# Optimization experiments

Measured on AMD Instinct MI355X. Metric: run time of the kernel, lower is better.

Reference implementation:

```python
import jax, jax.numpy as jnp
import numpy as np

K = 512
DIM = 64


def setup_inputs() -> dict:
    key = jax.random.key(0)
    kx, ke = jax.random.split(key)
    x = jax.random.normal(kx, (64, 64, 32, 32), dtype=jnp.float32)  # (b, d, h, w)
    codebook = jax.random.normal(ke, (K, DIM), dtype=jnp.float32)  # nn.Embedding weight
    return {"x": x, "codebook": codebook}


def reference(x, codebook):
    b, d, h, w = x.shape
    # (b, d, h*w) -> (b, h*w, d)
    flat = jnp.transpose(x.reshape(b, d, h * w), (0, 2, 1))  # (b, n, d)
    x2 = jnp.sum(flat * flat, axis=-1, keepdims=True)              # (b, n, 1)
    e2 = jnp.sum(codebook * codebook, axis=-1)                     # (k,)
    xe = jnp.einsum('bnd,kd->bnk', flat, codebook)                 # (b, n, k)
    dist = x2 - 2.0 * xe + e2                                      # (b, n, k)
    idx = jnp.argmin(dist, axis=-1)                                # (b, n)
    quant = codebook[idx]                                          # (b, n, d) gather
    # straight-through estimator
    quant_st = flat + jax.lax.stop_gradient(quant - flat)
    out = jnp.transpose(quant_st, (0, 2, 1)).reshape(b, d, h, w)
    return out
```

## Files before the change

kernel.cpp:

```cpp
#include <hip/hip_runtime.h>

#define KCODES 512
#define DIM    64
#define NVEC   65536
#define TAU    0.05f

typedef __attribute__((ext_vector_type(8))) short   short8;
typedef __attribute__((ext_vector_type(4))) float   f32x4;

static __device__ __forceinline__ unsigned f2bfu(float f) {
    unsigned u = __builtin_bit_cast(unsigned, f);
    u += 0x7fffu + ((u >> 16) & 1u);
    return u >> 16;
}

__global__ void prep_kernel(const float* __restrict__ cb,
                            unsigned short* __restrict__ cbh,
                            unsigned short* __restrict__ cbl,
                            float* __restrict__ e2q) {
    const int k = blockIdx.x, d = threadIdx.x;
    const int e = k * DIM + d;
    float v = cb[e];
    unsigned u = __builtin_bit_cast(unsigned, v);
    float hi = __builtin_bit_cast(float, u & 0xFFFF0000u);
    cbh[e] = (unsigned short)(u >> 16);
    cbl[e] = (unsigned short)f2bfu(v - hi);
    double p = (double)v * (double)v;
#pragma unroll
    for (int off = 32; off > 0; off >>= 1) p += __shfl_down(p, off, 64);
    if (d == 0) e2q[k] = (float)(0.5 * p + 256.0);
}

__launch_bounds__(128, 2)
__global__ void vq_main(const float* __restrict__ x,
                        const float* __restrict__ cb,
                        const unsigned short* __restrict__ cbh,
                        const unsigned short* __restrict__ cbl,
                        const float* __restrict__ e2q,
                        float* __restrict__ out) {
    __shared__ unsigned short sAh[2][4096];
    __shared__ unsigned short sAl[2][4096];
    __shared__ float sE2[KCODES];
    __shared__ int   s_i1[64], s_i2[64], s_flag[64], s_win[64];

    const int tid  = threadIdx.x;
    const int wave = tid >> 6;
    const int lane = tid & 63;
    const int quad = lane >> 4;
    const int l16  = lane & 15;

    const int v0    = blockIdx.x * 64;
    const int b     = v0 >> 10;
    const int nbase = v0 & 1023;
    const float* xb = x + (size_t)b * 65536;

    short8 stg[8];
#pragma unroll
    for (int r = 0; r < 8; ++r) {
        const int idx = tid + r * 128;
        const int q  = idx & 511;
        const int c  = q >> 3, qd = q & 7;
        const unsigned short* src = (idx < 512 ? cbh : cbl) + (size_t)c * 64 + qd * 8;
        stg[r] = *(const short8*)src;
    }

    short8 Bh[2][2], Bl[2][2];
#pragma unroll
    for (int nt = 0; nt < 2; ++nt) {
        const int n_g = nbase + wave * 32 + nt * 16 + l16;
#pragma unroll
        for (int ko = 0; ko < 2; ++ko) {
#pragma unroll
            for (int j = 0; j < 8; ++j) {
                const int d = quad * 8 + j + ko * 32;
                float f = -xb[(size_t)d * 1024 + n_g];
                unsigned u = __builtin_bit_cast(unsigned, f);
                float hi = __builtin_bit_cast(float, u & 0xFFFF0000u);
                Bh[nt][ko][j] = (short)(u >> 16);
                Bl[nt][ko][j] = (short)f2bfu(f - hi);
            }
        }
    }

    *(f32x4*)(sE2 + tid * 4) = *(const f32x4*)(e2q + tid * 4);
#pragma unroll
    for (int r = 0; r < 8; ++r) {
        const int idx = tid + r * 128;
        const int q  = idx & 511;
        const int c  = q >> 3, qd = q & 7;
        unsigned short* dst = (idx < 512 ? sAh[0] : sAl[0]) + (qd * 64 + c) * 8;
        *(short8*)dst = stg[r];
    }
    __syncthreads();

    float f1[2] = {1e30f, 1e30f}, f2_[2] = {1e30f, 1e30f};
    int   i1[2] = {0, 0},         i2_[2] = {0, 0};

#pragma unroll 1
    for (int s = 0; s < 8; ++s) {
        if (s < 7) {
#pragma unroll
            for (int r = 0; r < 8; ++r) {
                const int idx = tid + r * 128;
                const int q  = idx & 511;
                const int c  = q >> 3, qd = q & 7;
                const unsigned short* src =
                    (idx < 512 ? cbh : cbl) + (size_t)((s + 1) * 64 + c) * 64 + qd * 8;
                stg[r] = *(const short8*)src;
            }
        }

        const unsigned short* bh = sAh[s & 1];
        const unsigned short* bl = sAl[s & 1];
#pragma unroll
        for (int st = 0; st < 4; ++st) {
            const int cbase = s * 64 + st * 16;
            short8 Ah0 = *(const short8*)(bh + ( quad      * 64 + st * 16 + l16) * 8);
            short8 Ah1 = *(const short8*)(bh + ((quad + 4) * 64 + st * 16 + l16) * 8);
            short8 Al0 = *(const short8*)(bl + ( quad      * 64 + st * 16 + l16) * 8);
            short8 Al1 = *(const short8*)(bl + ((quad + 4) * 64 + st * 16 + l16) * 8);
            f32x4  e2v = *(const f32x4*)(sE2 + cbase + quad * 4);

#pragma unroll
            for (int nt = 0; nt < 2; ++nt) {
                f32x4 acc = e2v;
                acc = __builtin_amdgcn_mfma_f32_16x16x32_bf16(Ah0, Bh[nt][0], acc, 0, 0, 0);
                acc = __builtin_amdgcn_mfma_f32_16x16x32_bf16(Ah1, Bh[nt][1], acc, 0, 0, 0);
                acc = __builtin_amdgcn_mfma_f32_16x16x32_bf16(Ah0, Bl[nt][0], acc, 0, 0, 0);
                acc = __builtin_amdgcn_mfma_f32_16x16x32_bf16(Ah1, Bl[nt][1], acc, 0, 0, 0);
                acc = __builtin_amdgcn_mfma_f32_16x16x32_bf16(Al0, Bh[nt][0], acc, 0, 0, 0);
                acc = __builtin_amdgcn_mfma_f32_16x16x32_bf16(Al1, Bh[nt][1], acc, 0, 0, 0);
#pragma unroll
                for (int r = 0; r < 4; ++r) {
                    float dd = acc[r];
                    int   id = cbase + quad * 4 + r;
                    bool  c1 = dd < f1[nt];
                    bool  c2 = dd < f2_[nt];
                    i2_[nt] = c1 ? i1[nt] : (c2 ? id : i2_[nt]);
                    f2_[nt] = fminf(fmaxf(f1[nt], dd), f2_[nt]);
                    i1[nt]  = c1 ? id : i1[nt];
                    f1[nt]  = fminf(f1[nt], dd);
                }
            }
        }

        if (s < 7) {
#pragma unroll
            for (int r = 0; r < 8; ++r) {
                const int idx = tid + r * 128;
                const int q  = idx & 511;
                const int c  = q >> 3, qd = q & 7;
                unsigned short* dst =
                    (idx < 512 ? sAh[(s + 1) & 1] : sAl[(s + 1) & 1]) + (qd * 64 + c) * 8;
                *(short8*)dst = stg[r];
            }
        }
        __syncthreads();
    }

#pragma unroll
    for (int nt = 0; nt < 2; ++nt) {
        float F1 = f1[nt], F2 = f2_[nt];
        int   I1 = i1[nt], I2 = i2_[nt];
#pragma unroll
        for (int delta = 16; delta <= 32; delta <<= 1) {
            float of1 = __shfl_xor(F1, delta, 64);
            int   oi1 = __shfl_xor(I1, delta, 64);
            float of2 = __shfl_xor(F2, delta, 64);
            int   oi2 = __shfl_xor(I2, delta, 64);
            bool o1_first = (of1 < F1) || (of1 == F1 && oi1 < I1);
            if (o1_first) {
                bool keep = (F1 < of2) || (F1 == of2 && I1 < oi2);
                F2 = keep ? F1 : of2;
                I2 = keep ? I1 : oi2;
                F1 = of1; I1 = oi1;
            } else {
                bool o1_second = (of1 < F2) || (of1 == F2 && oi1 < I2);
                if (o1_second) { F2 = of1; I2 = oi1; }
            }
        }
        if (quad == 0) {
            const int vl = wave * 32 + nt * 16 + l16;
            s_win[vl]  = I1;
            s_i1[vl]   = I1;
            s_i2[vl]   = I2;
            s_flag[vl] = (F2 - F1) < TAU;
        }
    }
    __syncthreads();

    {
        const int vec = tid >> 1, sub = tid & 1;
        if (s_flag[vec]) {
            const int i1c = s_i1[vec], i2c = s_i2[vec];
            const float* xr = xb + nbase + vec;
            const float* r1 = cb + (size_t)i1c * DIM;
            const float* r2 = cb + (size_t)i2c * DIM;
            double D1 = 0.0, D2 = 0.0;
#pragma unroll 4
            for (int i = 0; i < 32; ++i) {
                const int d = sub + 2 * i;
                double xd = (double)xr[(size_t)d * 1024];
                double t1 = xd - (double)r1[d]; D1 += t1 * t1;
                double t2 = xd - (double)r2[d]; D2 += t2 * t2;
            }
            D1 += __shfl_down(D1, 1, 64);
            D2 += __shfl_down(D2, 1, 64);
            if (sub == 0) {
                if (D2 < D1 || (D2 == D1 && i2c < i1c)) s_win[vec] = i2c;
            }
        }
    }
    __syncthreads();

    {
        const int n    = tid & 63;
        const int dgrp = tid >> 6;
        const float4* crow = (const float4*)(cb + (size_t)s_win[n] * DIM);
        float* op = out + (size_t)b * 65536 + nbase + n;
#pragma unroll
        for (int i = 0; i < 8; ++i) {
            const int d0 = dgrp * 32 + i * 4;
            float4 val = crow[d0 >> 2];
            op[(size_t)(d0 + 0) * 1024] = val.x;
            op[(size_t)(d0 + 1) * 1024] = val.y;
            op[(size_t)(d0 + 2) * 1024] = val.z;
            op[(size_t)(d0 + 3) * 1024] = val.w;
        }
    }
}

extern "C" void kernel_launch(void* const* d_in, const int* in_sizes, int n_in,
                              void* d_out, int out_size, void* d_ws, size_t ws_size,
                              hipStream_t stream) {
    const float* x  = (const float*)d_in[0];
    const float* cb = (const float*)d_in[1];
    float* out = (float*)d_out;

    unsigned short* cbh = (unsigned short*)d_ws;
    unsigned short* cbl = cbh + KCODES * DIM;
    float*          e2q = (float*)(cbl + KCODES * DIM);

    prep_kernel<<<KCODES, 64, 0, stream>>>(cb, cbh, cbl, e2q);
    vq_main<<<NVEC / 64, 128, 0, stream>>>(x, cb, cbh, cbl, e2q, out);
}
```

Baseline: 106.6 us.

## Pre-tile codebook in LDS order and use four waves per 64-vector block

The prep kernel now writes the bf16 hi/lo codebook directly in the shared-memory tile order, so the main kernel stages it with plain contiguous 16-byte copies and no index shuffling. The main kernel goes from 128 to 256 threads per block, with each wave handling one 16-vector tile instead of two. Codebook staging, the refinement pass and the output write are split across the four waves. This is meant to raise the number of resident waves and spread the staging cost, at the price of each wave reusing its A-fragment LDS reads across fewer MFMAs.

```diff
diff --git a/kernel.cpp b/kernel.cpp
--- a/kernel.cpp
+++ b/kernel.cpp
@@ -15,31 +15,46 @@
 }
 
 __global__ void prep_kernel(const float* __restrict__ cb,
-                            unsigned short* __restrict__ cbh,
-                            unsigned short* __restrict__ cbl,
+                            unsigned short* __restrict__ cbt,
                             float* __restrict__ e2q) {
-    const int k = blockIdx.x, d = threadIdx.x;
-    const int e = k * DIM + d;
-    float v = cb[e];
-    unsigned u = __builtin_bit_cast(unsigned, v);
-    float hi = __builtin_bit_cast(float, u & 0xFFFF0000u);
-    cbh[e] = (unsigned short)(u >> 16);
-    cbl[e] = (unsigned short)f2bfu(v - hi);
-    double p = (double)v * (double)v;
-#pragma unroll
-    for (int off = 32; off > 0; off >>= 1) p += __shfl_down(p, off, 64);
-    if (d == 0) e2q[k] = (float)(0.5 * p + 256.0);
-}
-
-__launch_bounds__(128, 2)
+    if (blockIdx.x < 128) {
+        const int g   = blockIdx.x * 64 + threadIdx.x;
+        const int s   = g >> 10;
+        const int rem = g & 1023;
+        const int h   = rem >> 9;
+        const int qd  = (rem >> 6) & 7;
+        const int cl  = rem & 63;
+        const float* src = cb + (size_t)(s * 64 + cl) * DIM + qd * 8;
+        short8 v;
+#pragma unroll
+        for (int j = 0; j < 8; ++j) {
+            float f = src[j];
+            unsigned u = __builtin_bit_cast(unsigned, f);
+            if (h == 0) {
+                v[j] = (short)(u >> 16);
+            } else {
+                float hi = __builtin_bit_cast(float, u & 0xFFFF0000u);
+                v[j] = (short)f2bfu(f - hi);
+            }
+        }
+        *(short8*)(cbt + (size_t)g * 8) = v;
+    } else {
+        const int k = blockIdx.x - 128;
+        float v = cb[k * DIM + threadIdx.x];
+        double p = (double)v * (double)v;
+#pragma unroll
+        for (int off = 32; off > 0; off >>= 1) p += __shfl_down(p, off, 64);
+        if (threadIdx.x == 0) e2q[k] = (float)(0.5 * p + 256.0);
+    }
+}
+
+__launch_bounds__(256, 4)
 __global__ void vq_main(const float* __restrict__ x,
                         const float* __restrict__ cb,
-                        const unsigned short* __restrict__ cbh,
-                        const unsigned short* __restrict__ cbl,
+                        const unsigned short* __restrict__ cbt,
                         const float* __restrict__ e2q,
                         float* __restrict__ out) {
-    __shared__ unsigned short sAh[2][4096];
-    __shared__ unsigned short sAl[2][4096];
+    __shared__ __align__(16) unsigned short sA[2][8192];
     __shared__ float sE2[KCODES];
     __shared__ int   s_i1[64], s_i2[64], s_flag[64], s_win[64];
 
@@ -54,20 +69,14 @@
     const int nbase = v0 & 1023;
     const float* xb = x + (size_t)b * 65536;
 
-    short8 stg[8];
-#pragma unroll
-    for (int r = 0; r < 8; ++r) {
-        const int idx = tid + r * 128;
-        const int q  = idx & 511;
-        const int c  = q >> 3, qd = q & 7;
-        const unsigned short* src = (idx < 512 ? cbh : cbl) + (size_t)c * 64 + qd * 8;
-        stg[r] = *(const short8*)src;
-    }
-
-    short8 Bh[2][2], Bl[2][2];
-#pragma unroll
-    for (int nt = 0; nt < 2; ++nt) {
-        const int n_g = nbase + wave * 32 + nt * 16 + l16;
+    short8 stg[4];
+#pragma unroll
+    for (int r = 0; r < 4; ++r)
+        stg[r] = *(const short8*)(cbt + (size_t)(tid + r * 256) * 8);
+
+    short8 Bh[2], Bl[2];
+    {
+        const int n_g = nbase + wave * 16 + l16;
 #pragma unroll
         for (int ko = 0; ko < 2; ++ko) {
 #pragma unroll
@@ -76,121 +85,100 @@
                 float f = -xb[(size_t)d * 1024 + n_g];
                 unsigned u = __builtin_bit_cast(unsigned, f);
                 float hi = __builtin_bit_cast(float, u & 0xFFFF0000u);
-                Bh[nt][ko][j] = (short)(u >> 16);
-                Bl[nt][ko][j] = (short)f2bfu(f - hi);
-            }
-        }
-    }
-
-    *(f32x4*)(sE2 + tid * 4) = *(const f32x4*)(e2q + tid * 4);
-#pragma unroll
-    for (int r = 0; r < 8; ++r) {
-        const int idx = tid + r * 128;
-        const int q  = idx & 511;
-        const int c  = q >> 3, qd = q & 7;
-        unsigned short* dst = (idx < 512 ? sAh[0] : sAl[0]) + (qd * 64 + c) * 8;
-        *(short8*)dst = stg[r];
-    }
+                Bh[ko][j] = (short)(u >> 16);
+                Bl[ko][j] = (short)f2bfu(f - hi);
+            }
+        }
+    }
+
+    if (tid < 128) *(f32x4*)(sE2 + tid * 4) = *(const f32x4*)(e2q + tid * 4);
+#pragma unroll
+    for (int r = 0; r < 4; ++r)
+        *(short8*)(sA[0] + (size_t)(tid + r * 256) * 8) = stg[r];
     __syncthreads();
 
-    float f1[2] = {1e30f, 1e30f}, f2_[2] = {1e30f, 1e30f};
-    int   i1[2] = {0, 0},         i2_[2] = {0, 0};
+    float f1 = 1e30f, f2_ = 1e30f;
+    int   i1 = 0,     i2_ = 0;
 
 #pragma unroll 1
     for (int s = 0; s < 8; ++s) {
         if (s < 7) {
 #pragma unroll
-            for (int r = 0; r < 8; ++r) {
-                const int idx = tid + r * 128;
-                const int q  = idx & 511;
-                const int c  = q >> 3, qd = q & 7;
-                const unsigned short* src =
-                    (idx < 512 ? cbh : cbl) + (size_t)((s + 1) * 64 + c) * 64 + qd * 8;
-                stg[r] = *(const short8*)src;
-            }
-        }
-
-        const unsigned short* bh = sAh[s & 1];
-        const unsigned short* bl = sAl[s & 1];
+            for (int r = 0; r < 4; ++r)
+                stg[r] = *(const short8*)(cbt +
+                          (size_t)((s + 1) * 1024 + tid + r * 256) * 8);
+        }
+
+        const unsigned short* buf = sA[s & 1];
 #pragma unroll
         for (int st = 0; st < 4; ++st) {
             const int cbase = s * 64 + st * 16;
-            short8 Ah0 = *(const short8*)(bh + ( quad      * 64 + st * 16 + l16) * 8);
-            short8 Ah1 = *(const short8*)(bh + ((quad + 4) * 64 + st * 16 + l16) * 8);
-            short8 Al0 = *(const short8*)(bl + ( quad      * 64 + st * 16 + l16) * 8);
-            short8 Al1 = *(const short8*)(bl + ((quad + 4) * 64 + st * 16 + l16) * 8);
+            const int roff  = quad * 64 + st * 16 + l16;
+            short8 A00 = *(const short8*)(buf + (size_t)(      roff) * 8);
+            short8 A01 = *(const short8*)(buf + (size_t)(256 + roff) * 8);
+            short8 A10 = *(const short8*)(buf + (size_t)(512 + roff) * 8);
+            short8 A11 = *(const short8*)(buf + (size_t)(768 + roff) * 8);
             f32x4  e2v = *(const f32x4*)(sE2 + cbase + quad * 4);
 
-#pragma unroll
-            for (int nt = 0; nt < 2; ++nt) {
-                f32x4 acc = e2v;
-                acc = __builtin_amdgcn_mfma_f32_16x16x32_bf16(Ah0, Bh[nt][0], acc, 0, 0, 0);
-                acc = __builtin_amdgcn_mfma_f32_16x16x32_bf16(Ah1, Bh[nt][1], acc, 0, 0, 0);
-                acc = __builtin_amdgcn_mfma_f32_16x16x32_bf16(Ah0, Bl[nt][0], acc, 0, 0, 0);
-                acc = __builtin_amdgcn_mfma_f32_16x16x32_bf16(Ah1, Bl[nt][1], acc, 0, 0, 0);
-                acc = __builtin_amdgcn_mfma_f32_16x16x32_bf16(Al0, Bh[nt][0], acc, 0, 0, 0);
-                acc = __builtin_amdgcn_mfma_f32_16x16x32_bf16(Al1, Bh[nt][1], acc, 0, 0, 0);
-#pragma unroll
-                for (int r = 0; r < 4; ++r) {
-                    float dd = acc[r];
-                    int   id = cbase + quad * 4 + r;
-                    bool  c1 = dd < f1[nt];
-                    bool  c2 = dd < f2_[nt];
-                    i2_[nt] = c1 ? i1[nt] : (c2 ? id : i2_[nt]);
-                    f2_[nt] = fminf(fmaxf(f1[nt], dd), f2_[nt]);
-                    i1[nt]  = c1 ? id : i1[nt];
-                    f1[nt]  = fminf(f1[nt], dd);
-                }
+            f32x4 acc = e2v;
+            acc = __builtin_amdgcn_mfma_f32_16x16x32_bf16(A00, Bh[0], acc, 0, 0, 0);
+            acc = __builtin_amdgcn_mfma_f32_16x16x32_bf16(A01, Bh[1], acc, 0, 0, 0);
+            acc = __builtin_amdgcn_mfma_f32_16x16x32_bf16(A00, Bl[0], acc, 0, 0, 0);
+            acc = __builtin_amdgcn_mfma_f32_16x16x32_bf16(A01, Bl[1], acc, 0, 0, 0);
+            acc = __builtin_amdgcn_mfma_f32_16x16x32_bf16(A10, Bh[0], acc, 0, 0, 0);
+            acc = __builtin_amdgcn_mfma_f32_16x16x32_bf16(A11, Bh[1], acc, 0, 0, 0);
+
+#pragma unroll
+            for (int r = 0; r < 4; ++r) {
+                float dd = acc[r];
+                int   id = cbase + quad * 4 + r;
+                bool  c1 = dd < f1;
+                bool  c2 = dd < f2_;
+                i2_ = c1 ? i1 : (c2 ? id : i2_);
+                f2_ = fminf(fmaxf(f1, dd), f2_);
+                i1  = c1 ? id : i1;
+                f1  = fminf(f1, dd);
             }
         }
 
         if (s < 7) {
 #pragma unroll
-            for (int r = 0; r < 8; ++r) {
-                const int idx = tid + r * 128;
-                const int q  = idx & 511;
-                const int c  = q >> 3, qd = q & 7;
-                unsigned short* dst =
-                    (idx < 512 ? sAh[(s + 1) & 1] : sAl[(s + 1) & 1]) + (qd * 64 + c) * 8;
-                *(short8*)dst = stg[r];
-            }
+            for (int r = 0; r < 4; ++r)
+                *(short8*)(sA[(s + 1) & 1] + (size_t)(tid + r * 256) * 8) = stg[r];
         }
         __syncthreads();
     }
 
-#pragma unroll
-    for (int nt = 0; nt < 2; ++nt) {
-        float F1 = f1[nt], F2 = f2_[nt];
-        int   I1 = i1[nt], I2 = i2_[nt];
+    {
 #pragma unroll
         for (int delta = 16; delta <= 32; delta <<= 1) {
-            float of1 = __shfl_xor(F1, delta, 64);
-            int   oi1 = __shfl_xor(I1, delta, 64);
-            float of2 = __shfl_xor(F2, delta, 64);
-            int   oi2 = __shfl_xor(I2, delta, 64);
-            bool o1_first = (of1 < F1) || (of1 == F1 && oi1 < I1);
+            float of1 = __shfl_xor(f1, delta, 64);
+            int   oi1 = __shfl_xor(i1, delta, 64);
+            float of2 = __shfl_xor(f2_, delta, 64);
+            int   oi2 = __shfl_xor(i2_, delta, 64);
+            bool o1_first = (of1 < f1) || (of1 == f1 && oi1 < i1);
             if (o1_first) {
-                bool keep = (F1 < of2) || (F1 == of2 && I1 < oi2);
-                F2 = keep ? F1 : of2;
-                I2 = keep ? I1 : oi2;
-                F1 = of1; I1 = oi1;
+                bool keep = (f1 < of2) || (f1 == of2 && i1 < oi2);
+                f2_ = keep ? f1 : of2;
+                i2_ = keep ? i1 : oi2;
+                f1 = of1; i1 = oi1;
             } else {
-                bool o1_second = (of1 < F2) || (of1 == F2 && oi1 < I2);
-                if (o1_second) { F2 = of1; I2 = oi1; }
+                bool o1_second = (of1 < f2_) || (of1 == f2_ && oi1 < i2_);
+                if (o1_second) { f2_ = of1; i2_ = oi1; }
             }
         }
         if (quad == 0) {
-            const int vl = wave * 32 + nt * 16 + l16;
-            s_win[vl]  = I1;
-            s_i1[vl]   = I1;
-            s_i2[vl]   = I2;
-            s_flag[vl] = (F2 - F1) < TAU;
+            const int vl = wave * 16 + l16;
+            s_win[vl]  = i1;
+            s_i1[vl]   = i1;
+            s_i2[vl]   = i2_;
+            s_flag[vl] = (f2_ - f1) < TAU;
         }
     }
     __syncthreads();
 
     {
-        const int vec = tid >> 1, sub = tid & 1;
+        const int vec = tid >> 2, sub = tid & 3;
         if (s_flag[vec]) {
             const int i1c = s_i1[vec], i2c = s_i2[vec];
             const float* xr = xb + nbase + vec;
@@ -198,14 +186,14 @@
             const float* r2 = cb + (size_t)i2c * DIM;
             double D1 = 0.0, D2 = 0.0;
 #pragma unroll 4
-            for (int i = 0; i < 32; ++i) {
-                const int d = sub + 2 * i;
+            for (int i = 0; i < 16; ++i) {
+                const int d = sub + 4 * i;
                 double xd = (double)xr[(size_t)d * 1024];
                 double t1 = xd - (double)r1[d]; D1 += t1 * t1;
                 double t2 = xd - (double)r2[d]; D2 += t2 * t2;
             }
-            D1 += __shfl_down(D1, 1, 64);
-            D2 += __shfl_down(D2, 1, 64);
+            D1 += __shfl_down(D1, 2, 64); D1 += __shfl_down(D1, 1, 64);
+            D2 += __shfl_down(D2, 2, 64); D2 += __shfl_down(D2, 1, 64);
             if (sub == 0) {
                 if (D2 < D1 || (D2 == D1 && i2c < i1c)) s_win[vec] = i2c;
             }
@@ -219,8 +207,8 @@
         const float4* crow = (const float4*)(cb + (size_t)s_win[n] * DIM);
         float* op = out + (size_t)b * 65536 + nbase + n;
 #pragma unroll
-        for (int i = 0; i < 8; ++i) {
-            const int d0 = dgrp * 32 + i * 4;
+        for (int i = 0; i < 4; ++i) {
+            const int d0 = dgrp * 16 + i * 4;
             float4 val = crow[d0 >> 2];
             op[(size_t)(d0 + 0) * 1024] = val.x;
             op[(size_t)(d0 + 1) * 1024] = val.y;
@@ -237,10 +225,9 @@
     const float* cb = (const float*)d_in[1];
     float* out = (float*)d_out;
 
-    unsigned short* cbh = (unsigned short*)d_ws;
-    unsigned short* cbl = cbh + KCODES * DIM;
-    float*          e2q = (float*)(cbl + KCODES * DIM);
-
-    prep_kernel<<<KCODES, 64, 0, stream>>>(cb, cbh, cbl, e2q);
-    vq_main<<<NVEC / 64, 128, 0, stream>>>(x, cb, cbh, cbl, e2q, out);
-}
+    unsigned short* cbt = (unsigned short*)d_ws;
+    float*          e2q = (float*)(cbt + 8192 * 8);
+
+    prep_kernel<<<640, 64, 0, stream>>>(cb, cbt, e2q);
+    vq_main<<<NVEC / 64, 256, 0, stream>>>(x, cb, cbt, e2q, out);
+}
```

New measurement: 90.94 us (median of 2 runs). 1.17x faster.
